# Kernel optimization log

Hardware: AMD Instinct MI355X
Metric: run time of the kernel (lower is better)

The kernel has to match this reference:

```python
import jax, jax.numpy as jnp
import numpy as np
from jax import lax

B, T, H = 2, 1024, 2048
NH, D = 8, 128          # heads, head_dim
P = NH * D              # projection size
K = 4                   # short conv kernel size
EPS = 1e-6
SCALE = D ** -0.5


def _causal_conv_silu(x, w):
    # x: (B,T,C); w: (C,K) depthwise causal conv followed by silu (ShortConvolution)
    C = w.shape[0]
    kern = jnp.transpose(w)[:, None, :]  # (K,1,C)
    y = lax.conv_general_dilated(x, kern, window_strides=(1,), padding=[(K - 1, 0)],
                                 dimension_numbers=('NWC', 'WIO', 'NWC'),
                                 feature_group_count=C)
    return jax.nn.silu(y)


def _l2norm(x):
    return x * jax.lax.rsqrt(jnp.sum(x * x, axis=-1, keepdims=True) + EPS)


def _forward(hidden_states, Wq, Wk, Wv, conv_q, conv_k, conv_v, A_log, dt_bias,
             Wfa, Wfb, Wb, Wga, Wgb, norm_weight, Wo):
    x = hidden_states                                # (B,T,H)
    q = _causal_conv_silu(x @ Wq.T, conv_q)          # (B,T,P)
    k = _causal_conv_silu(x @ Wk.T, conv_k)
    v = _causal_conv_silu(x @ Wv.T, conv_v)
    # fused_kda_gate: g = -exp(A_log) * softplus(f_b(f_a(x)) + dt_bias), per (h,d) channel
    gf = (x @ Wfa.T) @ Wfb.T                         # (B,T,P) low-rank gate proj
    gf = gf.reshape(B, T, NH, D) + dt_bias.reshape(NH, D)
    g = -jnp.exp(A_log)[None, None, :, None] * jax.nn.softplus(gf)  # (B,T,NH,D) log-decay <= 0
    beta = jax.nn.sigmoid(x @ Wb.T)                  # (B,T,NH)
    q = _l2norm(q.reshape(B, T, NH, D)) * SCALE      # use_qk_l2norm_in_kernel + 1/sqrt(d) scale
    k = _l2norm(k.reshape(B, T, NH, D))
    v = v.reshape(B, T, NH, D)

    # gated delta-rule recurrence (KDA): per-key-channel decay, beta-weighted delta update
    def step(S, inp):
        q_t, k_t, v_t, g_t, b_t = inp                # (B,NH,D), beta (B,NH)
        S = S * jnp.exp(g_t)[..., None]              # decay rows (key dim) of S[.,.,dk,dv]
        kv = jnp.einsum('bhk,bhkv->bhv', k_t, S)
        delta = (v_t - kv) * b_t[..., None]
        S = S + jnp.einsum('bhk,bhv->bhkv', k_t, delta)
        o_t = jnp.einsum('bhk,bhkv->bhv', q_t, S)
        return S, o_t

    tfirst = lambda a: jnp.moveaxis(a, 1, 0)         # time-major for scan
    S0 = jnp.zeros((B, NH, D, D), x.dtype)
    _, o = lax.scan(step, S0, (tfirst(q), tfirst(k), tfirst(v), tfirst(g), tfirst(beta)))
    o = jnp.moveaxis(o, 0, 1)                        # (B,T,NH,D)

    # FusedRMSNormGated(sigmoid): gate applied before RMS normalization (Mamba2 convention)
    gate = ((x @ Wga.T) @ Wgb.T).reshape(B, T, NH, D)
    og = o * jax.nn.sigmoid(gate)
    og = og * jax.lax.rsqrt(jnp.mean(og * og, axis=-1, keepdims=True) + EPS) * norm_weight
    return og.reshape(B * T, P) @ Wo.T               # (B*T, H)


def setup_inputs():
    ks = jax.random.split(jax.random.key(0), 16)
    s = 0.02
    f32 = jnp.float32
    return {
        'hidden_states': jax.random.normal(ks[0], (B, T, H), f32),
        'Wq': jax.random.normal(ks[1], (P, H), f32) * s,
        'Wk': jax.random.normal(ks[2], (P, H), f32) * s,
        'Wv': jax.random.normal(ks[3], (P, H), f32) * s,
        'conv_q': jax.random.normal(ks[4], (P, K), f32) * 0.3,
        'conv_k': jax.random.normal(ks[5], (P, K), f32) * 0.3,
        'conv_v': jax.random.normal(ks[6], (P, K), f32) * 0.3,
        'A_log': jnp.log(jax.random.uniform(ks[7], (NH,), f32, 1.0, 16.0)),
        'dt_bias': jax.random.normal(ks[8], (P,), f32) * 0.5,
        'Wfa': jax.random.normal(ks[9], (D, H), f32) * s,
        'Wfb': jax.random.normal(ks[10], (P, D), f32) * s,
        'Wb': jax.random.normal(ks[11], (NH, H), f32) * s,
        'Wga': jax.random.normal(ks[12], (D, H), f32) * s,
        'Wgb': jax.random.normal(ks[13], (P, D), f32) * s,
        'norm_weight': jnp.ones((D,), f32),
        'Wo': jax.random.normal(ks[14], (H, P), f32) * s,
    }


def reference(hidden_states, Wq, Wk, Wv, conv_q, conv_k, conv_v, A_log, dt_bias,
              Wfa, Wfb, Wb, Wga, Wgb, norm_weight, Wo):
    return _forward(hidden_states, Wq, Wk, Wv, conv_q, conv_k, conv_v, A_log, dt_bias,
                    Wfa, Wfb, Wb, Wga, Wgb, norm_weight, Wo)
```

## Files before the change

kernel.cpp:

```cpp
#include <hip/hip_runtime.h>
#include <hip/hip_bf16.h>
#include <cstddef>
#include <cstdint>

#define Bb 2
#define Tt 1024
#define Hh 2048
#define NHh 8
#define Dd 128
#define Pp (NHh * Dd)
#define NW 4224
#define Kk 4
#define EPSf 1e-6f
#define SCALEf 0.08838834764831845f
#define DVQ 16
#define CHUNK 8

typedef short bf16x8 __attribute__((ext_vector_type(8)));
typedef float f32x4 __attribute__((ext_vector_type(4)));
typedef float f32x2 __attribute__((ext_vector_type(2)));

template <int CTRL>
__device__ __forceinline__ float dpp_add(float x) {
  int yi = __builtin_amdgcn_update_dpp(0, __builtin_bit_cast(int, x), CTRL, 0xF, 0xF, true);
  return x + __builtin_bit_cast(float, yi);
}
__device__ __forceinline__ float row16_sum(float x) {
  x = dpp_add<0xB1>(x);
  x = dpp_add<0x4E>(x);
  x = dpp_add<0x124>(x);
  x = dpp_add<0x128>(x);
  return x;
}

__device__ __forceinline__ void gload_lds16(const void* g, void* l) {
  __builtin_amdgcn_global_load_lds((const __attribute__((address_space(1))) void*)g,
                                   (__attribute__((address_space(3))) void*)l, 16, 0, 0);
}

__global__ __launch_bounds__(256) void cvt_bf16(const float* __restrict__ src,
                                                __hip_bfloat16* __restrict__ dst, int n) {
  const int i = (blockIdx.x * 256 + threadIdx.x) * 8;
  if (i >= n) return;
  const float4 a = *reinterpret_cast<const float4*>(src + i);
  const float4 b = *reinterpret_cast<const float4*>(src + i + 4);
  __hip_bfloat16 t[8];
  t[0] = __float2bfloat16(a.x); t[1] = __float2bfloat16(a.y);
  t[2] = __float2bfloat16(a.z); t[3] = __float2bfloat16(a.w);
  t[4] = __float2bfloat16(b.x); t[5] = __float2bfloat16(b.y);
  t[6] = __float2bfloat16(b.z); t[7] = __float2bfloat16(b.w);
  *reinterpret_cast<uint4*>(dst + i) = *reinterpret_cast<const uint4*>(t);
}

__global__ __launch_bounds__(256) void cvt_bf16_x4(const float* __restrict__ s0,
                                                   const float* __restrict__ s1,
                                                   const float* __restrict__ s2,
                                                   const float* __restrict__ s3,
                                                   __hip_bfloat16* __restrict__ d0,
                                                   __hip_bfloat16* __restrict__ d1,
                                                   __hip_bfloat16* __restrict__ d2,
                                                   __hip_bfloat16* __restrict__ d3,
                                                   int nper) {
  const int bpa = nper / 2048;
  const int a = blockIdx.x / bpa;
  const int i = (blockIdx.x % bpa) * 2048 + threadIdx.x * 8;
  const float* src = (a == 0) ? s0 : (a == 1) ? s1 : (a == 2) ? s2 : s3;
  __hip_bfloat16* dst = (a == 0) ? d0 : (a == 1) ? d1 : (a == 2) ? d2 : d3;
  const float4 x = *reinterpret_cast<const float4*>(src + i);
  const float4 y = *reinterpret_cast<const float4*>(src + i + 4);
  __hip_bfloat16 t[8];
  t[0] = __float2bfloat16(x.x); t[1] = __float2bfloat16(x.y);
  t[2] = __float2bfloat16(x.z); t[3] = __float2bfloat16(x.w);
  t[4] = __float2bfloat16(y.x); t[5] = __float2bfloat16(y.y);
  t[6] = __float2bfloat16(y.z); t[7] = __float2bfloat16(y.w);
  *reinterpret_cast<uint4*>(dst + i) = *reinterpret_cast<const uint4*>(t);
}

__global__ __launch_bounds__(256) void cvt_split(const float* __restrict__ src,
                                                 __hip_bfloat16* __restrict__ hi,
                                                 __hip_bfloat16* __restrict__ lo, int n) {
  const int i = (blockIdx.x * 256 + threadIdx.x) * 8;
  if (i >= n) return;
  __hip_bfloat16 th[8], tl[8];
#pragma unroll
  for (int j = 0; j < 2; j++) {
    const float4 a = *reinterpret_cast<const float4*>(src + i + j * 4);
    const float f[4] = {a.x, a.y, a.z, a.w};
#pragma unroll
    for (int e = 0; e < 4; e++) {
      const __hip_bfloat16 h = __float2bfloat16(f[e]);
      th[j * 4 + e] = h;
      tl[j * 4 + e] = __float2bfloat16(f[e] - __bfloat162float(h));
    }
  }
  *reinterpret_cast<uint4*>(hi + i) = *reinterpret_cast<const uint4*>(th);
  *reinterpret_cast<uint4*>(lo + i) = *reinterpret_cast<const uint4*>(tl);
}

__global__ __launch_bounds__(256) void gemm_nn_split(const float* __restrict__ A,
                                                     const float* __restrict__ B,
                                                     __hip_bfloat16* __restrict__ Chi,
                                                     __hip_bfloat16* __restrict__ Clo,
                                                     int M, int N, int K, int mode) {
  __shared__ float As[64][33];
  __shared__ float Bs[32][65];
  const int bm = blockIdx.y * 64, bn = blockIdx.x * 64;
  const int tid = threadIdx.x;
  const int tx = tid & 15, ty = tid >> 4;
  float acc[4][4];
#pragma unroll
  for (int i = 0; i < 4; i++)
#pragma unroll
    for (int j = 0; j < 4; j++) acc[i][j] = 0.f;
  for (int k0 = 0; k0 < K; k0 += 32) {
#pragma unroll
    for (int i = 0; i < 8; i++) {
      const int idx = tid + i * 256;
      const int r = idx >> 5, c = idx & 31;
      As[r][c] = A[(size_t)(bm + r) * K + k0 + c];
    }
#pragma unroll
    for (int i = 0; i < 8; i++) {
      const int idx = tid + i * 256;
      const int r = idx >> 6, c = idx & 63;
      Bs[r][c] = B[(size_t)(k0 + r) * N + bn + c];
    }
    __syncthreads();
#pragma unroll
    for (int kk = 0; kk < 32; kk++) {
      float a[4], b[4];
#pragma unroll
      for (int i = 0; i < 4; i++) a[i] = As[ty * 4 + i][kk];
#pragma unroll
      for (int j = 0; j < 4; j++) b[j] = Bs[kk][tx * 4 + j];
#pragma unroll
      for (int i = 0; i < 4; i++)
#pragma unroll
        for (int j = 0; j < 4; j++) acc[i][j] += a[i] * b[j];
    }
    __syncthreads();
  }
#pragma unroll
  for (int i = 0; i < 4; i++) {
    const int row = bm + ty * 4 + i;
#pragma unroll
    for (int j = 0; j < 4; j++) {
      const int col = bn + tx * 4 + j;
      const float v = acc[i][j];
      const __hip_bfloat16 h = __float2bfloat16(v);
      Chi[(size_t)row * N + col] = h;
      if (mode == 0) Clo[(size_t)row * N + col] = __float2bfloat16(v - __bfloat162float(h));
    }
  }
}

__global__ __launch_bounds__(256) void gemm_bf16_lds(const __hip_bfloat16* __restrict__ A,
                                                     const __hip_bfloat16* __restrict__ B,
                                                     float* __restrict__ C,
                                                     __hip_bfloat16* __restrict__ Cbf,
                                                     int M, int N, int K, int outmode) {
  __shared__ __align__(16) __hip_bfloat16 As[128 * 64];
  __shared__ __align__(16) __hip_bfloat16 Bs[128 * 64];
  const int tid = threadIdx.x;
  const int wave = tid >> 6;
  const int lane = tid & 63;
  const int wm = (wave >> 1) * 64;
  const int wn = (wave & 1) * 64;
  const int bm = blockIdx.y * 128;
  const int bn = blockIdx.x * 128;
  const int l15 = lane & 15;
  const int l4 = lane >> 4;
  const int srow = lane >> 3;
  const int scol = (lane & 7) * 8;

  f32x4 acc[4][4];
#pragma unroll
  for (int i = 0; i < 4; i++)
#pragma unroll
    for (int j = 0; j < 4; j++) acc[i][j] = (f32x4){0.f, 0.f, 0.f, 0.f};

  for (int k0 = 0; k0 < K; k0 += 64) {
#pragma unroll
    for (int i = 0; i < 4; i++) {
      const int s = wave * 4 + i;
      const int row = s * 8 + srow;
      gload_lds16(A + (size_t)(bm + row) * K + k0 + scol, &As[s * 512]);
      gload_lds16(B + (size_t)(bn + row) * K + k0 + scol, &Bs[s * 512]);
    }
    __syncthreads();
    bf16x8 af[4][2], bfv[4][2];
#pragma unroll
    for (int kf = 0; kf < 2; kf++) {
      const int kc = kf * 32 + l4 * 8;
#pragma unroll
      for (int mf = 0; mf < 4; mf++)
        af[mf][kf] = *reinterpret_cast<const bf16x8*>(&As[(wm + mf * 16 + l15) * 64 + kc]);
#pragma unroll
      for (int nf = 0; nf < 4; nf++)
        bfv[nf][kf] = *reinterpret_cast<const bf16x8*>(&Bs[(wn + nf * 16 + l15) * 64 + kc]);
    }
#pragma unroll
    for (int kf = 0; kf < 2; kf++)
#pragma unroll
      for (int mf = 0; mf < 4; mf++)
#pragma unroll
        for (int nf = 0; nf < 4; nf++)
          acc[mf][nf] = __builtin_amdgcn_mfma_f32_16x16x32_bf16(af[mf][kf], bfv[nf][kf],
                                                                acc[mf][nf], 0, 0, 0);
    __syncthreads();
  }
#pragma unroll
  for (int mf = 0; mf < 4; mf++) {
#pragma unroll
    for (int nf = 0; nf < 4; nf++) {
      const int col = bn + wn + nf * 16 + l15;
#pragma unroll
      for (int r = 0; r < 4; r++) {
        const int row = bm + wm + mf * 16 + l4 * 4 + r;
        if (outmode == 0) C[(size_t)row * N + col] = acc[mf][nf][r];
        else Cbf[(size_t)row * N + col] = __float2bfloat16(acc[mf][nf][r]);
      }
    }
  }
}

__global__ __launch_bounds__(256) void gemm_bf16_3t_lds(const __hip_bfloat16* __restrict__ Ahi,
                                                        const __hip_bfloat16* __restrict__ Alo,
                                                        const __hip_bfloat16* __restrict__ Bhi,
                                                        const __hip_bfloat16* __restrict__ Blo,
                                                        float* __restrict__ C,
                                                        int M, int N, int K,
                                                        const float* __restrict__ dtb,
                                                        const float* __restrict__ A_log,
                                                        int gmode) {
  __shared__ __align__(16) __hip_bfloat16 Ahs[64 * 64];
  __shared__ __align__(16) __hip_bfloat16 Als[64 * 64];
  __shared__ __align__(16) __hip_bfloat16 Bhs[128 * 64];
  __shared__ __align__(16) __hip_bfloat16 Bls[128 * 64];
  const int tid = threadIdx.x;
  const int wave = tid >> 6;
  const int lane = tid & 63;
  const int wm = (wave >> 1) * 32;
  const int wn = (wave & 1) * 64;
  const int bm = blockIdx.y * 64;
  const int bn = blockIdx.x * 128;
  const int l15 = lane & 15;
  const int l4 = lane >> 4;
  const int srow = lane >> 3;
  const int scol = (lane & 7) * 8;

  f32x4 acc[2][4];
#pragma unroll
  for (int i = 0; i < 2; i++)
#pragma unroll
    for (int j = 0; j < 4; j++) acc[i][j] = (f32x4){0.f, 0.f, 0.f, 0.f};

  for (int k0 = 0; k0 < K; k0 += 64) {
#pragma unroll
    for (int i = 0; i < 12; i++) {
      const int sid = wave * 12 + i;
      if (sid < 8) {
        const int row = sid * 8 + srow;
        gload_lds16(Ahi + (size_t)(bm + row) * K + k0 + scol, &Ahs[sid * 512]);
      } else if (sid < 16) {
        const int row = (sid - 8) * 8 + srow;
        gload_lds16(Alo + (size_t)(bm + row) * K + k0 + scol, &Als[(sid - 8) * 512]);
      } else if (sid < 32) {
        const int row = (sid - 16) * 8 + srow;
        gload_lds16(Bhi + (size_t)(bn + row) * K + k0 + scol, &Bhs[(sid - 16) * 512]);
      } else {
        const int row = (sid - 32) * 8 + srow;
        gload_lds16(Blo + (size_t)(bn + row) * K + k0 + scol, &Bls[(sid - 32) * 512]);
      }
    }
    __syncthreads();
#pragma unroll
    for (int kf = 0; kf < 2; kf++) {
      const int kc = kf * 32 + l4 * 8;
      bf16x8 ah[2], al[2], bh[4], bl[4];
#pragma unroll
      for (int mf = 0; mf < 2; mf++) {
        ah[mf] = *reinterpret_cast<const bf16x8*>(&Ahs[(wm + mf * 16 + l15) * 64 + kc]);
        al[mf] = *reinterpret_cast<const bf16x8*>(&Als[(wm + mf * 16 + l15) * 64 + kc]);
      }
#pragma unroll
      for (int nf = 0; nf < 4; nf++) {
        bh[nf] = *reinterpret_cast<const bf16x8*>(&Bhs[(wn + nf * 16 + l15) * 64 + kc]);
        bl[nf] = *reinterpret_cast<const bf16x8*>(&Bls[(wn + nf * 16 + l15) * 64 + kc]);
      }
#pragma unroll
      for (int mf = 0; mf < 2; mf++)
#pragma unroll
        for (int nf = 0; nf < 4; nf++) {
          acc[mf][nf] = __builtin_amdgcn_mfma_f32_16x16x32_bf16(ah[mf], bh[nf], acc[mf][nf], 0, 0, 0);
          acc[mf][nf] = __builtin_amdgcn_mfma_f32_16x16x32_bf16(ah[mf], bl[nf], acc[mf][nf], 0, 0, 0);
          acc[mf][nf] = __builtin_amdgcn_mfma_f32_16x16x32_bf16(al[mf], bh[nf], acc[mf][nf], 0, 0, 0);
        }
    }
    __syncthreads();
  }
#pragma unroll
  for (int mf = 0; mf < 2; mf++)
#pragma unroll
    for (int nf = 0; nf < 4; nf++) {
      const int col = bn + wn + nf * 16 + l15;
#pragma unroll
      for (int r = 0; r < 4; r++) {
        const int row = bm + wm + mf * 16 + l4 * 4 + r;
        float val = acc[mf][nf][r];
        if (gmode) {
          const float xv = val + dtb[col];
          const float sp = (xv > 20.f) ? xv : log1pf(expf(xv));
          val = expf(-expf(A_log[col >> 7]) * sp);
        }
        C[(size_t)row * N + col] = val;
      }
    }
}

__global__ __launch_bounds__(256) void gemm_nt(const float* __restrict__ A,
                                               const float* __restrict__ Bm,
                                               float* __restrict__ C,
                                               int M, int N, int Kd) {
  __shared__ float As[16][64];
  __shared__ float Bs[16][64];
  const int bm = blockIdx.y * 64;
  const int bn = blockIdx.x * 64;
  const int tid = threadIdx.x;
  const int tx = tid & 15;
  const int ty = tid >> 4;
  const int lr = tid >> 2;
  const int lc = (tid & 3) << 2;
  float acc[4][4];
#pragma unroll
  for (int i = 0; i < 4; i++)
#pragma unroll
    for (int j = 0; j < 4; j++) acc[i][j] = 0.f;
  for (int k0 = 0; k0 < Kd; k0 += 16) {
    float4 a4 = make_float4(0.f, 0.f, 0.f, 0.f);
    float4 b4 = make_float4(0.f, 0.f, 0.f, 0.f);
    const int ar = bm + lr;
    if (ar < M) a4 = *reinterpret_cast<const float4*>(A + (size_t)ar * Kd + k0 + lc);
    const int br = bn + lr;
    if (br < N) b4 = *reinterpret_cast<const float4*>(Bm + (size_t)br * Kd + k0 + lc);
    As[lc + 0][lr] = a4.x; As[lc + 1][lr] = a4.y; As[lc + 2][lr] = a4.z; As[lc + 3][lr] = a4.w;
    Bs[lc + 0][lr] = b4.x; Bs[lc + 1][lr] = b4.y; Bs[lc + 2][lr] = b4.z; Bs[lc + 3][lr] = b4.w;
    __syncthreads();
#pragma unroll
    for (int kk = 0; kk < 16; kk++) {
      float4 av = *reinterpret_cast<const float4*>(&As[kk][ty << 2]);
      float4 bv = *reinterpret_cast<const float4*>(&Bs[kk][tx << 2]);
      float a[4] = {av.x, av.y, av.z, av.w};
      float b[4] = {bv.x, bv.y, bv.z, bv.w};
#pragma unroll
      for (int i = 0; i < 4; i++)
#pragma unroll
        for (int j = 0; j < 4; j++) acc[i][j] += a[i] * b[j];
    }
    __syncthreads();
  }
#pragma unroll
  for (int i = 0; i < 4; i++) {
    const int row = bm + (ty << 2) + i;
    if (row >= M) continue;
#pragma unroll
    for (int j = 0; j < 4; j++) {
      const int col = bn + (tx << 2) + j;
      if (col < N) C[(size_t)row * N + col] = acc[i][j];
    }
  }
}

__global__ __launch_bounds__(256) void beta_kernel(const float* __restrict__ x,
                                                   const float* __restrict__ Wb,
                                                   float* __restrict__ beta) {
  __shared__ float xs[Hh];
  const int m = blockIdx.x;
  const int tid = threadIdx.x;
  for (int i = tid; i < Hh; i += 256) xs[i] = x[(size_t)m * Hh + i];
  __syncthreads();
  const int h = tid >> 5;
  const int lane = tid & 31;
  float acc = 0.f;
  for (int i = lane; i < Hh; i += 32) acc += xs[i] * Wb[(size_t)h * Hh + i];
#pragma unroll
  for (int o = 16; o > 0; o >>= 1) acc += __shfl_down(acc, o, 32);
  if (lane == 0) beta[(size_t)m * NHh + h] = 1.f / (1.f + expf(-acc));
}

__global__ __launch_bounds__(256) void g_kernel(float* __restrict__ gbuf,
                                                const float* __restrict__ dtb,
                                                const float* __restrict__ A_log) {
  const size_t i = (size_t)blockIdx.x * 256 + threadIdx.x;
  const int c = (int)(i % Pp);
  const int h = c / Dd;
  const float xv = gbuf[i] + dtb[c];
  const float sp = (xv > 20.f) ? xv : log1pf(expf(xv));
  gbuf[i] = expf(-expf(A_log[h]) * sp);
}

__global__ __launch_bounds__(128) void conv_silu_norm(const float* __restrict__ xin,
                                                      const float* __restrict__ w,
                                                      float* __restrict__ out,
                                                      int mode, int instride, int coff) {
  const int idx = blockIdx.x;
  const int h = idx % NHh;
  const int bt = idx / NHh;
  const int t = bt % Tt;
  const int d = threadIdx.x;
  const int c = h * Dd + d;
  float acc = 0.f;
#pragma unroll
  for (int j = 0; j < Kk; j++) {
    const int tt = t - (Kk - 1) + j;
    float xv = 0.f;
    if (tt >= 0) xv = xin[(size_t)(bt - (Kk - 1) + j) * instride + coff + c];
    acc += w[c * Kk + j] * xv;
  }
  float y = acc / (1.f + expf(-acc));
  float r = y;
  if (mode > 0) {
    float ss = y * y;
#pragma unroll
    for (int o = 32; o > 0; o >>= 1) ss += __shfl_down(ss, o);
    __shared__ float red[2];
    if ((d & 63) == 0) red[d >> 6] = ss;
    __syncthreads();
    const float tot = red[0] + red[1];
    const float inv = rsqrtf(tot + EPSf);
    r = y * inv * (mode == 2 ? SCALEf : 1.f);
  }
  out[(size_t)bt * Pp + c] = r;
}

__global__ __launch_bounds__(128) void conv3_kernel(const float* __restrict__ qkvpre,
                                                    const float* __restrict__ cq,
                                                    const float* __restrict__ ck,
                                                    const float* __restrict__ cv,
                                                    float* __restrict__ outbase,
                                                    int instride) {
  const int nblk = Bb * Tt * NHh;
  const int which = blockIdx.x / nblk;
  const int idx = blockIdx.x % nblk;
  const float* w = (which == 0) ? cq : (which == 1) ? ck : cv;
  const int mode = (which == 0) ? 2 : (which == 1) ? 1 : 0;
  const int h = idx % NHh;
  const int bt = idx / NHh;
  const int t = bt % Tt;
  const int d = threadIdx.x;
  const int c = h * Dd + d;
  float acc = 0.f;
#pragma unroll
  for (int j = 0; j < Kk; j++) {
    const int tt = t - (Kk - 1) + j;
    float xv = 0.f;
    if (tt >= 0) xv = qkvpre[(size_t)(bt - (Kk - 1) + j) * instride + which * Pp + c];
    acc += w[c * Kk + j] * xv;
  }
  float y = acc / (1.f + expf(-acc));
  float r = y;
  if (mode > 0) {
    float ss = y * y;
#pragma unroll
    for (int o = 32; o > 0; o >>= 1) ss += __shfl_down(ss, o);
    __shared__ float red[2];
    if ((d & 63) == 0) red[d >> 6] = ss;
    __syncthreads();
    const float tot = red[0] + red[1];
    const float inv = rsqrtf(tot + EPSf);
    r = y * inv * (mode == 2 ? SCALEf : 1.f);
  }
  outbase[(size_t)which * (Bb * Tt) * Pp + (size_t)bt * Pp + c] = r;
}

__global__ __launch_bounds__(128) void scan_kernel(const float* __restrict__ q,
                                                   const float* __restrict__ k,
                                                   const float* __restrict__ v,
                                                   const float* __restrict__ eg,
                                                   const float* __restrict__ betasrc,
                                                   int bstride, int bcol, int bsig,
                                                   float* __restrict__ o) {
  const int blk = blockIdx.x;
  const int bh = blk & 15;
  const int dvq = blk >> 4;
  const int b = bh >> 3, h = bh & 7;
  const int tid = threadIdx.x;
  const int qr = tid & 15;
  const int dvl = tid >> 4;
  const int dv = dvq * 8 + dvl;

  __shared__ __align__(16) float qs[2][CHUNK][16][12];
  __shared__ __align__(16) float ks[2][CHUNK][16][12];
  __shared__ __align__(16) float legs[2][CHUNK][16][12];
  __shared__ float vs[2][CHUNK][8];
  __shared__ float betas[2][CHUNK];

  f32x2 s2[4];
#pragma unroll
  for (int i = 0; i < 4; i++) s2[i] = (f32x2){0.f, 0.f};

  const size_t base = (size_t)(b * Tt) * Pp + h * Dd;
  const int le = tid;

  float rq[CHUNK], rk[CHUNK], re[CHUNK], rv[CHUNK], rb = 0.f;
  auto load_chunk = [&](int t0) {
    const size_t coff = base + (size_t)t0 * Pp;
#pragma unroll
    for (int j = 0; j < CHUNK; j++) {
      rq[j] = q[coff + (size_t)j * Pp + le];
      rk[j] = k[coff + (size_t)j * Pp + le];
      re[j] = eg[coff + (size_t)j * Pp + le];
    }
    if (tid < 8) {
#pragma unroll
      for (int j = 0; j < CHUNK; j++) rv[j] = v[coff + (size_t)j * Pp + dvq * 8 + tid];
    } else if (tid < 8 + CHUNK) {
      const float brw = betasrc[(size_t)(b * Tt + t0 + tid - 8) * bstride + bcol + h];
      rb = bsig ? 1.f / (1.f + expf(-brw)) : brw;
    }
  };
  auto write_lds = [&](int bufw) {
#pragma unroll
    for (int j = 0; j < CHUNK; j++) {
      qs[bufw][j][le >> 3][le & 7] = rq[j];
      ks[bufw][j][le >> 3][le & 7] = rk[j];
      legs[bufw][j][le >> 3][le & 7] = re[j];
    }
    if (tid < 8) {
#pragma unroll
      for (int j = 0; j < CHUNK; j++) vs[bufw][j][tid] = rv[j];
    } else if (tid < 8 + CHUNK) {
      betas[bufw][tid - 8] = rb;
    }
  };
  auto unpack = [](const float4& a, const float4& b, f32x2 out[4]) {
    out[0] = (f32x2){a.x, a.y}; out[1] = (f32x2){a.z, a.w};
    out[2] = (f32x2){b.x, b.y}; out[3] = (f32x2){b.z, b.w};
  };

  load_chunk(0);
  write_lds(0);
  __syncthreads();
  const int NC = Tt / CHUNK;
  size_t off = base;
  for (int c = 0; c < NC; c++) {
    if (c + 1 < NC) load_chunk((c + 1) * CHUNK);
    const int buf = c & 1;
    float vv[CHUNK], bb[CHUNK], opart[CHUNK];
#pragma unroll
    for (int j = 0; j < CHUNK; j++) { vv[j] = vs[buf][j][dvl]; bb[j] = betas[buf][j]; }

    f32x2 ck2[4], ce2[4], cq2[4], kt2[4];
    {
      const float4 k0 = *reinterpret_cast<const float4*>(&ks[buf][0][qr][0]);
      const float4 k1 = *reinterpret_cast<const float4*>(&ks[buf][0][qr][4]);
      const float4 e0 = *reinterpret_cast<const float4*>(&legs[buf][0][qr][0]);
      const float4 e1 = *reinterpret_cast<const float4*>(&legs[buf][0][qr][4]);
      const float4 q0 = *reinterpret_cast<const float4*>(&qs[buf][0][qr][0]);
      const float4 q1 = *reinterpret_cast<const float4*>(&qs[buf][0][qr][4]);
      unpack(k0, k1, ck2); unpack(e0, e1, ce2); unpack(q0, q1, cq2);
#pragma unroll
      for (int i = 0; i < 4; i++) kt2[i] = ck2[i] * ce2[i];
    }

#pragma unroll
    for (int j = 0; j < CHUNK; j++) {
      float4 nk0, nk1, ne0, ne1, nq0, nq1;
      if (j + 1 < CHUNK) {
        nk0 = *reinterpret_cast<const float4*>(&ks[buf][j + 1][qr][0]);
        nk1 = *reinterpret_cast<const float4*>(&ks[buf][j + 1][qr][4]);
        ne0 = *reinterpret_cast<const float4*>(&legs[buf][j + 1][qr][0]);
        ne1 = *reinterpret_cast<const float4*>(&legs[buf][j + 1][qr][4]);
        nq0 = *reinterpret_cast<const float4*>(&qs[buf][j + 1][qr][0]);
        nq1 = *reinterpret_cast<const float4*>(&qs[buf][j + 1][qr][4]);
      }
      f32x2 es0 = ce2[0] * s2[0], es1 = ce2[1] * s2[1];
      f32x2 es2v = ce2[2] * s2[2], es3 = ce2[3] * s2[3];
      f32x2 kva = kt2[0] * s2[0];
      f32x2 kvb = kt2[1] * s2[1];
      kva = kt2[2] * s2[2] + kva;
      kvb = kt2[3] * s2[3] + kvb;
      kva = kva + kvb;
      const float kvp = row16_sum(kva.x + kva.y);
      const float delta = (vv[j] - kvp) * bb[j];
      const f32x2 d2 = (f32x2){delta, delta};
      f32x2 o2;
      s2[0] = ck2[0] * d2 + es0;  o2 = cq2[0] * s2[0];
      s2[1] = ck2[1] * d2 + es1;  o2 = cq2[1] * s2[1] + o2;
      s2[2] = ck2[2] * d2 + es2v; o2 = cq2[2] * s2[2] + o2;
      s2[3] = ck2[3] * d2 + es3;  o2 = cq2[3] * s2[3] + o2;
      opart[j] = o2.x + o2.y;
      if (j + 1 < CHUNK) {
        unpack(nk0, nk1, ck2); unpack(ne0, ne1, ce2); unpack(nq0, nq1, cq2);
#pragma unroll
        for (int i = 0; i < 4; i++) kt2[i] = ck2[i] * ce2[i];
      }
    }
#pragma unroll
    for (int j = 0; j < CHUNK; j++) opart[j] = row16_sum(opart[j]);
    if (qr == 0) {
#pragma unroll
      for (int j = 0; j < CHUNK; j++) o[off + (size_t)j * Pp + dv] = opart[j];
    }
    if (c + 1 < NC) write_lds(buf ^ 1);
    __syncthreads();
    off += (size_t)CHUNK * Pp;
  }
}

__global__ __launch_bounds__(128) void gated_norm(float* __restrict__ o,
                                                  const float* __restrict__ gate,
                                                  int gstride,
                                                  const float* __restrict__ nw,
                                                  __hip_bfloat16* __restrict__ ogbf) {
  const int idx = blockIdx.x;
  const int h = idx % NHh;
  const int bt = idx / NHh;
  const int d = threadIdx.x;
  const size_t off = (size_t)bt * Pp + h * Dd;
  const float ov = o[off + d];
  const float gt = gate[(size_t)bt * gstride + h * Dd + d];
  const float val = ov / (1.f + expf(-gt));
  float ss = val * val;
#pragma unroll
  for (int sh = 32; sh > 0; sh >>= 1) ss += __shfl_down(ss, sh);
  __shared__ float red[2];
  if ((d & 63) == 0) red[d >> 6] = ss;
  __syncthreads();
  const float mean = (red[0] + red[1]) * (1.f / Dd);
  const float res = val * rsqrtf(mean + EPSf) * nw[d];
  if (ogbf != nullptr) ogbf[off + d] = __float2bfloat16(res);
  else o[off + d] = res;
}

extern "C" void kernel_launch(void* const* d_in, const int* in_sizes, int n_in,
                              void* d_out, int out_size, void* d_ws, size_t ws_size,
                              hipStream_t stream) {
  const float* x     = (const float*)d_in[0];
  const float* Wq    = (const float*)d_in[1];
  const float* Wk    = (const float*)d_in[2];
  const float* Wv    = (const float*)d_in[3];
  const float* cq    = (const float*)d_in[4];
  const float* ck    = (const float*)d_in[5];
  const float* cv    = (const float*)d_in[6];
  const float* A_log = (const float*)d_in[7];
  const float* dtb   = (const float*)d_in[8];
  const float* Wfa   = (const float*)d_in[9];
  const float* Wfb   = (const float*)d_in[10];
  const float* Wb    = (const float*)d_in[11];
  const float* Wga   = (const float*)d_in[12];
  const float* Wgb   = (const float*)d_in[13];
  const float* nw    = (const float*)d_in[14];
  const float* Wo    = (const float*)d_in[15];
  float* outp = (float*)d_out;

  const int M = Bb * Tt;
  const size_t MP = (size_t)M * Pp;
  float* ws = (float*)d_ws;
  float* qkvpre = ws;
  float* qb   = qkvpre + (size_t)M * NW;
  float* kb   = qb + MP;
  float* vb   = kb + MP;
  float* gbuf = vb + MP;
  float* obuf = gbuf + MP;
  float* betab = obuf + MP;
  float* gfa  = betab + (size_t)M * NHh;
  float* gga  = gfa + (size_t)M * Dd;
  float* f32end = gga + (size_t)M * Dd;

  __hip_bfloat16* xhi    = (__hip_bfloat16*)f32end;
  __hip_bfloat16* xlo    = xhi + (size_t)M * Hh;
  __hip_bfloat16* Wqkvbf = xlo + (size_t)M * Hh;
  __hip_bfloat16* Wobf   = Wqkvbf + (size_t)NW * Hh;
  __hip_bfloat16* Wcombhi = Wobf + (size_t)Hh * Pp;
  __hip_bfloat16* Wcomblo = Wcombhi + (size_t)Pp * Hh;
  __hip_bfloat16* end = Wcomblo + (size_t)Pp * Hh;
  __hip_bfloat16* ogbf = xlo;
  const bool use_mfma = ws_size >= (size_t)((char*)end - (char*)d_ws);

  const dim3 blk(256);
  if (use_mfma) {
    cvt_split<<<(int)((size_t)M * Hh / 2048), blk, 0, stream>>>(x, xhi, xlo, M * Hh);
    cvt_bf16_x4<<<4 * (int)((size_t)Pp * Hh / 2048), blk, 0, stream>>>(
        Wq, Wk, Wv, Wo, Wqkvbf, Wqkvbf + (size_t)Pp * Hh, Wqkvbf + (size_t)2 * Pp * Hh,
        Wobf, Pp * Hh);
    cvt_bf16<<<(NHh * Hh) / 2048, blk, 0, stream>>>(Wb, Wqkvbf + (size_t)4096 * Hh, NHh * Hh);
    gemm_nn_split<<<dim3(Hh / 64, Pp / 64), blk, 0, stream>>>(Wfb, Wfa, Wcombhi, Wcomblo,
                                                              Pp, Hh, Dd, 0);
    gemm_nn_split<<<dim3(Hh / 64, Pp / 64), blk, 0, stream>>>(Wgb, Wga,
                                                              Wqkvbf + (size_t)3 * Pp * Hh,
                                                              nullptr, Pp, Hh, Dd, 1);
    gemm_bf16_lds<<<dim3(NW / 128, M / 128), blk, 0, stream>>>(xhi, Wqkvbf, qkvpre, nullptr,
                                                               M, NW, Hh, 0);
    gemm_bf16_3t_lds<<<dim3(Pp / 128, M / 64), blk, 0, stream>>>(xhi, xlo, Wcombhi, Wcomblo,
                                                                 gbuf, M, Pp, Hh,
                                                                 dtb, A_log, 1);
    conv3_kernel<<<3 * M * NHh, 128, 0, stream>>>(qkvpre, cq, ck, cv, qb, NW);
    scan_kernel<<<Bb * NHh * DVQ, 128, 0, stream>>>(qb, kb, vb, gbuf,
                                                    qkvpre, NW, 4096, 1, obuf);
    gated_norm<<<M * NHh, 128, 0, stream>>>(obuf, qkvpre + (size_t)3 * Pp, NW, nw, ogbf);
    gemm_bf16_lds<<<dim3(Hh / 128, M / 128), blk, 0, stream>>>(ogbf, Wobf, outp, nullptr,
                                                               M, Hh, Pp, 0);
  } else {
    float* qpre = qkvpre;
    float* kpre = qkvpre + MP;
    float* vpre = qkvpre + 2 * MP;
    float* gate = qkvpre + 3 * MP;
    gemm_nt<<<dim3(Pp / 64, M / 64), blk, 0, stream>>>(x, Wq, qpre, M, Pp, Hh);
    gemm_nt<<<dim3(Pp / 64, M / 64), blk, 0, stream>>>(x, Wk, kpre, M, Pp, Hh);
    gemm_nt<<<dim3(Pp / 64, M / 64), blk, 0, stream>>>(x, Wv, vpre, M, Pp, Hh);
    gemm_nt<<<dim3(Dd / 64, M / 64), blk, 0, stream>>>(x, Wfa, gfa, M, Dd, Hh);
    gemm_nt<<<dim3(Dd / 64, M / 64), blk, 0, stream>>>(x, Wga, gga, M, Dd, Hh);
    gemm_nt<<<dim3(Pp / 64, M / 64), blk, 0, stream>>>(gfa, Wfb, gbuf, M, Pp, Dd);
    gemm_nt<<<dim3(Pp / 64, M / 64), blk, 0, stream>>>(gga, Wgb, gate, M, Pp, Dd);
    beta_kernel<<<M, 256, 0, stream>>>(x, Wb, betab);
    g_kernel<<<(int)(MP / 256), 256, 0, stream>>>(gbuf, dtb, A_log);
    conv_silu_norm<<<M * NHh, 128, 0, stream>>>(qpre, cq, qb, 2, Pp, 0);
    conv_silu_norm<<<M * NHh, 128, 0, stream>>>(kpre, ck, kb, 1, Pp, 0);
    conv_silu_norm<<<M * NHh, 128, 0, stream>>>(vpre, cv, vb, 0, Pp, 0);
    scan_kernel<<<Bb * NHh * DVQ, 128, 0, stream>>>(qb, kb, vb, gbuf,
                                                    betab, NHh, 0, 0, obuf);
    gated_norm<<<M * NHh, 128, 0, stream>>>(obuf, gate, Pp, nw, nullptr);
    gemm_nt<<<dim3(Hh / 64, M / 64), blk, 0, stream>>>(obuf, Wo, outp, M, Hh, Pp);
  }
}
```

Measured before the change: 503.7 us.

## Process four timesteps per conv block and move beta projection out of QKV GEMM

```diff
diff --git a/kernel.cpp b/kernel.cpp
--- a/kernel.cpp
+++ b/kernel.cpp
@@ -9,7 +9,6 @@
 #define NHh 8
 #define Dd 128
 #define Pp (NHh * Dd)
-#define NW 4224
 #define Kk 4
 #define EPSf 1e-6f
 #define SCALEf 0.08838834764831845f
@@ -433,52 +432,65 @@
   out[(size_t)bt * Pp + c] = r;
 }
 
-__global__ __launch_bounds__(128) void conv3_kernel(const float* __restrict__ qkvpre,
-                                                    const float* __restrict__ cq,
-                                                    const float* __restrict__ ck,
-                                                    const float* __restrict__ cv,
-                                                    float* __restrict__ outbase,
-                                                    int instride) {
-  const int nblk = Bb * Tt * NHh;
-  const int which = blockIdx.x / nblk;
-  const int idx = blockIdx.x % nblk;
+__global__ __launch_bounds__(128) void conv3b_kernel(const float* __restrict__ qkvpre,
+                                                     const float* __restrict__ cq,
+                                                     const float* __restrict__ ck,
+                                                     const float* __restrict__ cv,
+                                                     float* __restrict__ outbase) {
+  const int nper = (Bb * Tt / 4) * NHh;
+  const int which = blockIdx.x / nper;
+  const int idx = blockIdx.x % nper;
   const float* w = (which == 0) ? cq : (which == 1) ? ck : cv;
   const int mode = (which == 0) ? 2 : (which == 1) ? 1 : 0;
   const int h = idx % NHh;
-  const int bt = idx / NHh;
-  const int t = bt % Tt;
+  const int bt0 = (idx / NHh) * 4;
+  const int t0 = bt0 % Tt;
   const int d = threadIdx.x;
   const int c = h * Dd + d;
-  float acc = 0.f;
-#pragma unroll
-  for (int j = 0; j < Kk; j++) {
-    const int tt = t - (Kk - 1) + j;
-    float xv = 0.f;
-    if (tt >= 0) xv = qkvpre[(size_t)(bt - (Kk - 1) + j) * instride + which * Pp + c];
-    acc += w[c * Kk + j] * xv;
-  }
-  float y = acc / (1.f + expf(-acc));
-  float r = y;
+
+  float xw[7];
+#pragma unroll
+  for (int i = 0; i < 7; i++) {
+    const int tt = t0 - 3 + i;
+    xw[i] = (tt >= 0) ? qkvpre[(size_t)(bt0 - 3 + i) * (4 * Pp) + which * Pp + c] : 0.f;
+  }
+  const float w0 = w[c * Kk + 0], w1 = w[c * Kk + 1], w2 = w[c * Kk + 2], w3 = w[c * Kk + 3];
+  float y[4];
+#pragma unroll
+  for (int jj = 0; jj < 4; jj++) {
+    const float a = w0 * xw[jj] + w1 * xw[jj + 1] + w2 * xw[jj + 2] + w3 * xw[jj + 3];
+    y[jj] = a / (1.f + expf(-a));
+  }
   if (mode > 0) {
-    float ss = y * y;
-#pragma unroll
-    for (int o = 32; o > 0; o >>= 1) ss += __shfl_down(ss, o);
-    __shared__ float red[2];
-    if ((d & 63) == 0) red[d >> 6] = ss;
-    __syncthreads();
-    const float tot = red[0] + red[1];
-    const float inv = rsqrtf(tot + EPSf);
-    r = y * inv * (mode == 2 ? SCALEf : 1.f);
-  }
-  outbase[(size_t)which * (Bb * Tt) * Pp + (size_t)bt * Pp + c] = r;
+    float ss[4];
+#pragma unroll
+    for (int jj = 0; jj < 4; jj++) ss[jj] = y[jj] * y[jj];
+#pragma unroll
+    for (int o = 32; o > 0; o >>= 1) {
+#pragma unroll
+      for (int jj = 0; jj < 4; jj++) ss[jj] += __shfl_down(ss[jj], o);
+    }
+    __shared__ float red[2][4];
+    if ((d & 63) == 0) {
+#pragma unroll
+      for (int jj = 0; jj < 4; jj++) red[d >> 6][jj] = ss[jj];
+    }
+    __syncthreads();
+    const float sc = (mode == 2) ? SCALEf : 1.f;
+#pragma unroll
+    for (int jj = 0; jj < 4; jj++)
+      y[jj] = y[jj] * rsqrtf(red[0][jj] + red[1][jj] + EPSf) * sc;
+  }
+  float* outp = outbase + (size_t)which * (Bb * Tt) * Pp;
+#pragma unroll
+  for (int jj = 0; jj < 4; jj++) outp[(size_t)(bt0 + jj) * Pp + c] = y[jj];
 }
 
 __global__ __launch_bounds__(128) void scan_kernel(const float* __restrict__ q,
                                                    const float* __restrict__ k,
                                                    const float* __restrict__ v,
                                                    const float* __restrict__ eg,
-                                                   const float* __restrict__ betasrc,
-                                                   int bstride, int bcol, int bsig,
+                                                   const float* __restrict__ beta,
                                                    float* __restrict__ o) {
   const int blk = blockIdx.x;
   const int bh = blk & 15;
@@ -515,8 +527,7 @@
 #pragma unroll
       for (int j = 0; j < CHUNK; j++) rv[j] = v[coff + (size_t)j * Pp + dvq * 8 + tid];
     } else if (tid < 8 + CHUNK) {
-      const float brw = betasrc[(size_t)(b * Tt + t0 + tid - 8) * bstride + bcol + h];
-      rb = bsig ? 1.f / (1.f + expf(-brw)) : brw;
+      rb = beta[(size_t)(b * Tt + t0 + tid - 8) * NHh + h];
     }
   };
   auto write_lds = [&](int bufw) {
@@ -658,7 +669,7 @@
   const size_t MP = (size_t)M * Pp;
   float* ws = (float*)d_ws;
   float* qkvpre = ws;
-  float* qb   = qkvpre + (size_t)M * NW;
+  float* qb   = qkvpre + 4 * MP;
   float* kb   = qb + MP;
   float* vb   = kb + MP;
   float* gbuf = vb + MP;
@@ -671,7 +682,7 @@
   __hip_bfloat16* xhi    = (__hip_bfloat16*)f32end;
   __hip_bfloat16* xlo    = xhi + (size_t)M * Hh;
   __hip_bfloat16* Wqkvbf = xlo + (size_t)M * Hh;
-  __hip_bfloat16* Wobf   = Wqkvbf + (size_t)NW * Hh;
+  __hip_bfloat16* Wobf   = Wqkvbf + (size_t)4 * Pp * Hh;
   __hip_bfloat16* Wcombhi = Wobf + (size_t)Hh * Pp;
   __hip_bfloat16* Wcomblo = Wcombhi + (size_t)Pp * Hh;
   __hip_bfloat16* end = Wcomblo + (size_t)Pp * Hh;
@@ -684,21 +695,20 @@
     cvt_bf16_x4<<<4 * (int)((size_t)Pp * Hh / 2048), blk, 0, stream>>>(
         Wq, Wk, Wv, Wo, Wqkvbf, Wqkvbf + (size_t)Pp * Hh, Wqkvbf + (size_t)2 * Pp * Hh,
         Wobf, Pp * Hh);
-    cvt_bf16<<<(NHh * Hh) / 2048, blk, 0, stream>>>(Wb, Wqkvbf + (size_t)4096 * Hh, NHh * Hh);
     gemm_nn_split<<<dim3(Hh / 64, Pp / 64), blk, 0, stream>>>(Wfb, Wfa, Wcombhi, Wcomblo,
                                                               Pp, Hh, Dd, 0);
     gemm_nn_split<<<dim3(Hh / 64, Pp / 64), blk, 0, stream>>>(Wgb, Wga,
                                                               Wqkvbf + (size_t)3 * Pp * Hh,
                                                               nullptr, Pp, Hh, Dd, 1);
-    gemm_bf16_lds<<<dim3(NW / 128, M / 128), blk, 0, stream>>>(xhi, Wqkvbf, qkvpre, nullptr,
-                                                               M, NW, Hh, 0);
+    gemm_bf16_lds<<<dim3(4 * Pp / 128, M / 128), blk, 0, stream>>>(xhi, Wqkvbf, qkvpre, nullptr,
+                                                                   M, 4 * Pp, Hh, 0);
     gemm_bf16_3t_lds<<<dim3(Pp / 128, M / 64), blk, 0, stream>>>(xhi, xlo, Wcombhi, Wcomblo,
                                                                  gbuf, M, Pp, Hh,
                                                                  dtb, A_log, 1);
-    conv3_kernel<<<3 * M * NHh, 128, 0, stream>>>(qkvpre, cq, ck, cv, qb, NW);
-    scan_kernel<<<Bb * NHh * DVQ, 128, 0, stream>>>(qb, kb, vb, gbuf,
-                                                    qkvpre, NW, 4096, 1, obuf);
-    gated_norm<<<M * NHh, 128, 0, stream>>>(obuf, qkvpre + (size_t)3 * Pp, NW, nw, ogbf);
+    beta_kernel<<<M, 256, 0, stream>>>(x, Wb, betab);
+    conv3b_kernel<<<3 * (M / 4) * NHh, 128, 0, stream>>>(qkvpre, cq, ck, cv, qb);
+    scan_kernel<<<Bb * NHh * DVQ, 128, 0, stream>>>(qb, kb, vb, gbuf, betab, obuf);
+    gated_norm<<<M * NHh, 128, 0, stream>>>(obuf, qkvpre + (size_t)3 * Pp, 4 * Pp, nw, ogbf);
     gemm_bf16_lds<<<dim3(Hh / 128, M / 128), blk, 0, stream>>>(ogbf, Wobf, outp, nullptr,
                                                                M, Hh, Pp, 0);
   } else {
@@ -718,8 +728,7 @@
     conv_silu_norm<<<M * NHh, 128, 0, stream>>>(qpre, cq, qb, 2, Pp, 0);
     conv_silu_norm<<<M * NHh, 128, 0, stream>>>(kpre, ck, kb, 1, Pp, 0);
     conv_silu_norm<<<M * NHh, 128, 0, stream>>>(vpre, cv, vb, 0, Pp, 0);
-    scan_kernel<<<Bb * NHh * DVQ, 128, 0, stream>>>(qb, kb, vb, gbuf,
-                                                    betab, NHh, 0, 0, obuf);
+    scan_kernel<<<Bb * NHh * DVQ, 128, 0, stream>>>(qb, kb, vb, gbuf, betab, obuf);
     gated_norm<<<M * NHh, 128, 0, stream>>>(obuf, gate, Pp, nw, nullptr);
     gemm_nt<<<dim3(Hh / 64, M / 64), blk, 0, stream>>>(obuf, Wo, outp, M, Hh, Pp);
   }
```

Result: faster. 446.4 us (median of 2 runs) (-11.4%).
